# Optimization experiments

Hardware: AMD Instinct MI355X
Metric: run time of the kernel (lower is better)

The kernel has to match this reference:

```python
import jax, jax.numpy as jnp
import numpy as np

N_NODE, N_NET, E = 100000, 20000, 200000
H_NODE, H_NET, H_PIN = 64, 32, 16
O_NODE, O_NET = 32, 64


def setup_inputs() -> dict:
    key = jax.random.key(0)
    ks = jax.random.split(key, 8)
    return {
        'node_feat': jax.random.normal(ks[0], (N_NODE, H_NODE), jnp.float32),
        'net_feat': jax.random.normal(ks[1], (N_NET, H_NET), jnp.float32),
        'pin_feat': jax.random.normal(ks[2], (E, H_PIN), jnp.float32),
        'edge_node': jax.random.randint(ks[3], (E,), 0, N_NODE, jnp.int32),
        'edge_net': jax.random.randint(ks[4], (E,), 0, N_NET, jnp.int32),
        'W1': jax.random.normal(ks[5], (H_NODE, O_NET), jnp.float32) * 0.05,
        'b1': jnp.zeros((O_NET,), jnp.float32),
        'W2': jax.random.normal(ks[6], (H_PIN, H_NET * O_NODE), jnp.float32) * 0.05,
        'b2': jnp.zeros((H_NET * O_NODE,), jnp.float32),
        'b_nn': jnp.zeros((O_NODE,), jnp.float32),
    }


def reference(node_feat, net_feat, pin_feat, edge_node, edge_net, W1, b1, W2, b2, b_nn):
    ones = jnp.ones((E,), node_feat.dtype)
    # ---- relation 'pins': node -> net, DGL GraphConv with norm='both' ----
    out_deg = jnp.clip(jax.ops.segment_sum(ones, edge_node, num_segments=N_NODE), 1.0)  # src out-degree
    in_deg = jnp.clip(jax.ops.segment_sum(ones, edge_net, num_segments=N_NET), 1.0)     # dst in-degree
    src = node_feat * jax.lax.rsqrt(out_deg)[:, None]                                   # [N_node, H_node]
    agg = jax.ops.segment_sum(src[edge_node], edge_net, num_segments=N_NET)             # [N_net, H_node]
    net_out = (agg * jax.lax.rsqrt(in_deg)[:, None]) @ W1 + b1                           # [N_net, O_net]
    # ---- relation 'pinned': net -> node, DGL NNConv (mean aggregator) ----
    We = (pin_feat @ W2 + b2).reshape(E, H_NET, O_NODE)                                  # per-edge weight matrix
    msg = jnp.einsum('ei,eio->eo', net_feat[edge_net], We)                               # [E, O_node]
    node_deg = jnp.clip(jax.ops.segment_sum(ones, edge_node, num_segments=N_NODE), 1.0)
    node_out = jax.ops.segment_sum(msg, edge_node, num_segments=N_NODE) / node_deg[:, None] + b_nn
    return node_out, net_out
```

## Files before the change

kernel.cpp:

```cpp
#include <hip/hip_runtime.h>
#include <hip/hip_bf16.h>

#define N_NODE 100000
#define N_NET  20000
#define NE     200000
#define H_NODE 64
#define H_NET  32
#define H_PIN  16
#define O_NODE 32
#define O_NET  64
#define CSR_STRIDE 64


#define OFF_NETCNT  400000
#define OFF_CSR     480000
#define OFF_Z       10720000
#define OFF_C       51680000
#define ZERO_BYTES  480000

#define FILL_EDGE_BLKS 782
#define FILL_INIT_BLKS 3125

__global__ void k_fill(const int* __restrict__ en, const int* __restrict__ em,
                       int* __restrict__ node_deg, int* __restrict__ net_cnt,
                       int2* __restrict__ csr,
                       const float* __restrict__ b_nn,
                       float* __restrict__ out_node) {
    int t = threadIdx.x, b = blockIdx.x;
    if (b < FILL_EDGE_BLKS) {
        int e = b * 256 + t;
        if (e < NE) {
            int v = en[e], n = em[e];
            atomicAdd(&node_deg[v], 1);
            int slot = atomicAdd(&net_cnt[n], 1);
            csr[n * CSR_STRIDE + slot] = make_int2(e, v);
        }
        return;
    }
    int idx = (b - FILL_EDGE_BLKS) * 256 + t;
    float4 bb = ((const float4*)b_nn)[idx & 7];
    ((float4*)out_node)[idx] = bb;
}

#define ZNPB 16
__global__ void k_pre(const float* __restrict__ net_feat,
                      const float* __restrict__ W2, const float* __restrict__ b2,
                      float* __restrict__ Z, float* __restrict__ C) {
    __shared__ float sy[ZNPB][H_NET];
    int t = threadIdx.x;
    int base = blockIdx.x * ZNPB;
    for (int idx = t; idx < ZNPB * H_NET; idx += 256)
        sy[idx >> 5][idx & 31] = net_feat[(base + (idx >> 5)) * H_NET + (idx & 31)];
    __syncthreads();
    int o = t & 31, k4 = (t >> 5) & 3, rep = t >> 7;
    const float* w2p = W2 + (k4 * 4) * 1024 + o;
    float4 acc[8];
#pragma unroll
    for (int g = 0; g < 8; g++) acc[g] = make_float4(0.f, 0.f, 0.f, 0.f);
#pragma unroll 4
    for (int i = 0; i < H_NET; i++) {
        float w0 = w2p[0 * 1024 + i * 32];
        float w1 = w2p[1 * 1024 + i * 32];
        float w2v = w2p[2 * 1024 + i * 32];
        float w3 = w2p[3 * 1024 + i * 32];
#pragma unroll
        for (int g = 0; g < 8; g++) {
            float y = sy[rep * 8 + g][i];
            acc[g].x += w0 * y; acc[g].y += w1 * y;
            acc[g].z += w2v * y; acc[g].w += w3 * y;
        }
    }
#pragma unroll
    for (int g = 0; g < 8; g++) {
        int n = base + rep * 8 + g;
        *(float4*)&Z[(size_t)n * 512 + o * 16 + k4 * 4] = acc[g];
    }
#pragma unroll
    for (int r = 0; r < 2; r++) {
        int idx = t + r * 256;
        int g = idx >> 5, oo = idx & 31;
        float a = 0.f;
#pragma unroll
        for (int i = 0; i < H_NET; i++) a += sy[g][i] * b2[i * 32 + oo];
        C[(base + g) * 32 + oo] = a;
    }
}

__global__ void k_net(const float* __restrict__ node_feat,
                      const int* __restrict__ node_deg,
                      const int* __restrict__ net_cnt,
                      const int2* __restrict__ csr,
                      const float* __restrict__ W1,
                      const float* __restrict__ b1,
                      const float* __restrict__ Zg,
                      const float* __restrict__ Cg,
                      const float* __restrict__ pin_feat,
                      float* __restrict__ out_net, float* __restrict__ out_node) {
    __shared__ float  sW1[H_NODE * O_NET];
    __shared__ float  spin[4][32][16];
    __shared__ float4 srow4[4][16];
    int t = threadIdx.x;
    for (int i = t; i < 1024; i += 256)
        ((float4*)sW1)[i] = ((const float4*)W1)[i];

    int w = t >> 6, l = t & 63;
    int n = blockIdx.x * 4 + w;
    int beg = n * CSR_STRIDE, deg = net_cnt[n];
    int o = l & 31;
    int half = l >> 5;
    int q = l >> 4, f = l & 15;

    float4 z4[4];
    {
        const float4* zp = (const float4*)&Zg[(size_t)n * 512 + o * 16];
#pragma unroll
        for (int k4 = 0; k4 < 4; k4++) z4[k4] = zp[k4];
    }
    float c = Cg[n * 32 + o];

    const float4* nf4 = (const float4*)node_feat;
    const float4* pf4 = (const float4*)pin_feat;

    float4 acc4 = make_float4(0.f, 0.f, 0.f, 0.f);

    for (int j0 = 0; j0 < deg; j0 += 32) {
        int cnt = deg - j0; if (cnt > 32) cnt = 32;
        int vj = 0, ej = 0; float sj = 0.f;
        if (l < cnt) {
            int2 ev = csr[beg + j0 + l];
            ej = ev.x; vj = ev.y;
            float dv = (float)node_deg[vj]; if (dv < 1.f) dv = 1.f;
            sj = rsqrtf(dv);
        }
#pragma unroll
        for (int r = 0; r < 2; r++) {
            int jj = r * 16 + (l >> 2);
            int src = (jj < cnt) ? jj : cnt - 1;
            int e = __shfl(ej, src);
            float4 pv = pf4[(size_t)e * 4 + (l & 3)];
            ((float4*)&spin[w][jj][0])[l & 3] = pv;
        }
        int   vv[8]; float ss[8];
#pragma unroll
        for (int r = 0; r < 8; r++) {
            int jj = r * 4 + q;
            int src = (jj < cnt) ? jj : cnt - 1;
            vv[r] = __shfl(vj, src);
            float sv = __shfl(sj, src);
            ss[r] = (jj < cnt) ? sv : 0.f;
        }
        float4 xx[8];
#pragma unroll
        for (int r = 0; r < 8; r++) xx[r] = nf4[(size_t)vv[r] * 16 + f];
#pragma unroll
        for (int r = 0; r < 8; r++) {
            acc4.x += xx[r].x * ss[r];
            acc4.y += xx[r].y * ss[r];
            acc4.z += xx[r].z * ss[r];
            acc4.w += xx[r].w * ss[r];
        }
        for (int jj = 0; jj < cnt; jj += 2) {
            int je = jj + half;
            int src = (je < cnt) ? je : cnt - 1;
            int v = __shfl(vj, src);
            float sv = __shfl(sj, src);
            float inv = sv * sv;
            const float4* pr = (const float4*)&spin[w][src][0];
            float m = c;
#pragma unroll
            for (int k4 = 0; k4 < 4; k4++) {
                float4 pv = pr[k4];
                m += pv.x * z4[k4].x + pv.y * z4[k4].y
                   + pv.z * z4[k4].z + pv.w * z4[k4].w;
            }
            if (je < cnt) atomicAdd(&out_node[(size_t)v * O_NODE + o], m * inv);
        }
    }
    acc4.x += __shfl_xor(acc4.x, 16); acc4.y += __shfl_xor(acc4.y, 16);
    acc4.z += __shfl_xor(acc4.z, 16); acc4.w += __shfl_xor(acc4.w, 16);
    acc4.x += __shfl_xor(acc4.x, 32); acc4.y += __shfl_xor(acc4.y, 32);
    acc4.z += __shfl_xor(acc4.z, 32); acc4.w += __shfl_xor(acc4.w, 32);
    float dn = (deg < 1) ? 1.f : (float)deg;
    float rs = rsqrtf(dn);
    if (l < 16)
        srow4[w][l] = make_float4(acc4.x * rs, acc4.y * rs, acc4.z * rs, acc4.w * rs);
    __syncthreads();
    {
        const float* a = (const float*)&srow4[w][0];
        float oacc = b1[l];
#pragma unroll
        for (int h = 0; h < H_NODE; h++) oacc += a[h] * sW1[h * O_NET + l];
        out_net[n * O_NET + l] = oacc;
    }
}

extern "C" void kernel_launch(void* const* d_in, const int* in_sizes, int n_in,
                              void* d_out, int out_size, void* d_ws, size_t ws_size,
                              hipStream_t stream) {
    const float* node_feat = (const float*)d_in[0];
    const float* net_feat  = (const float*)d_in[1];
    const float* pin_feat  = (const float*)d_in[2];
    const int*   edge_node = (const int*)d_in[3];
    const int*   edge_net  = (const int*)d_in[4];
    const float* W1        = (const float*)d_in[5];
    const float* b1        = (const float*)d_in[6];
    const float* W2        = (const float*)d_in[7];
    const float* b2        = (const float*)d_in[8];
    const float* b_nn      = (const float*)d_in[9];

    float* out_node = (float*)d_out;
    float* out_net  = out_node + (size_t)N_NODE * O_NODE;

    char* ws = (char*)d_ws;
    int*   node_deg = (int*)ws;
    int*   net_cnt  = (int*)(ws + OFF_NETCNT);
    int2*  csr      = (int2*)(ws + OFF_CSR);
    float* Z        = (float*)(ws + OFF_Z);
    float* C        = (float*)(ws + OFF_C);

    (void)hipMemsetAsync(ws, 0, ZERO_BYTES, stream);

    k_fill<<<FILL_EDGE_BLKS + FILL_INIT_BLKS, 256, 0, stream>>>(
        edge_node, edge_net, node_deg, net_cnt, csr, b_nn, out_node);

    k_pre<<<N_NET / ZNPB, 256, 0, stream>>>(net_feat, W2, b2, Z, C);

    k_net<<<N_NET / 4, 256, 0, stream>>>(
        node_feat, node_deg, net_cnt, csr,
        W1, b1, Z, C, pin_feat, out_net, out_node);
}
```

Measured before the change: 174.0 us.

## Fuse precompute into build kernel, store Z in bf16, trim W1 staging and gathers

Merges the Z/C precompute kernel into the CSR build kernel so one launch does all setup work. The per-net Z matrix is stored in bf16, halving its write and read traffic, which costs some precision in the per-edge messages. k_net drops the shared-memory staging of W1 and reads it directly from global memory. It also skips the second half of the pin and node gathers when a net has 16 or fewer edges.

New measurement: 163.7 us. -5.9%, faster.

```diff
diff --git a/kernel.cpp b/kernel.cpp
--- a/kernel.cpp
+++ b/kernel.cpp
@@ -15,75 +15,87 @@
 #define OFF_NETCNT  400000
 #define OFF_CSR     480000
 #define OFF_Z       10720000
-#define OFF_C       51680000
+#define OFF_C       31200000
 #define ZERO_BYTES  480000
 
-#define FILL_EDGE_BLKS 782
-#define FILL_INIT_BLKS 3125
-
-__global__ void k_fill(const int* __restrict__ en, const int* __restrict__ em,
-                       int* __restrict__ node_deg, int* __restrict__ net_cnt,
-                       int2* __restrict__ csr,
-                       const float* __restrict__ b_nn,
-                       float* __restrict__ out_node) {
+static __device__ __forceinline__ unsigned short f2bf(float f) {
+    unsigned int u = __float_as_uint(f);
+    u += 0x7fff + ((u >> 16) & 1);
+    return (unsigned short)(u >> 16);
+}
+static __device__ __forceinline__ float bf2f(unsigned short h) {
+    return __uint_as_float(((unsigned int)h) << 16);
+}
+
+#define BLD_EDGE_BLKS 782
+#define BLD_Z_BLKS    1250
+#define BLD_INIT_BLKS 3125
+#define ZNPB 16
+
+__global__ void k_build(const int* __restrict__ en, const int* __restrict__ em,
+                        int* __restrict__ node_deg, int* __restrict__ net_cnt,
+                        int2* __restrict__ csr,
+                        const float* __restrict__ net_feat,
+                        const float* __restrict__ W2, const float* __restrict__ b2,
+                        unsigned short* __restrict__ Zb, float* __restrict__ C,
+                        const float* __restrict__ b_nn,
+                        float* __restrict__ out_node) {
     int t = threadIdx.x, b = blockIdx.x;
-    if (b < FILL_EDGE_BLKS) {
+    if (b < BLD_EDGE_BLKS) {
         int e = b * 256 + t;
         if (e < NE) {
             int v = en[e], n = em[e];
             atomicAdd(&node_deg[v], 1);
             int slot = atomicAdd(&net_cnt[n], 1);
-            csr[n * CSR_STRIDE + slot] = make_int2(e, v);
+            if (slot < CSR_STRIDE) csr[n * CSR_STRIDE + slot] = make_int2(e, v);
         }
         return;
     }
-    int idx = (b - FILL_EDGE_BLKS) * 256 + t;
-    float4 bb = ((const float4*)b_nn)[idx & 7];
-    ((float4*)out_node)[idx] = bb;
-}
-
-#define ZNPB 16
-__global__ void k_pre(const float* __restrict__ net_feat,
-                      const float* __restrict__ W2, const float* __restrict__ b2,
-                      float* __restrict__ Z, float* __restrict__ C) {
-    __shared__ float sy[ZNPB][H_NET];
-    int t = threadIdx.x;
-    int base = blockIdx.x * ZNPB;
-    for (int idx = t; idx < ZNPB * H_NET; idx += 256)
-        sy[idx >> 5][idx & 31] = net_feat[(base + (idx >> 5)) * H_NET + (idx & 31)];
-    __syncthreads();
-    int o = t & 31, k4 = (t >> 5) & 3, rep = t >> 7;
-    const float* w2p = W2 + (k4 * 4) * 1024 + o;
-    float4 acc[8];
-#pragma unroll
-    for (int g = 0; g < 8; g++) acc[g] = make_float4(0.f, 0.f, 0.f, 0.f);
+    if (b < BLD_EDGE_BLKS + BLD_Z_BLKS) {
+        __shared__ float sy[ZNPB][H_NET];
+        int base = (b - BLD_EDGE_BLKS) * ZNPB;
+        for (int idx = t; idx < ZNPB * H_NET; idx += 256)
+            sy[idx >> 5][idx & 31] = net_feat[(base + (idx >> 5)) * H_NET + (idx & 31)];
+        __syncthreads();
+        int o = t & 31, k4 = (t >> 5) & 3, rep = t >> 7;
+        const float* w2p = W2 + (k4 * 4) * 1024 + o;
+        float4 acc[8];
+#pragma unroll
+        for (int g = 0; g < 8; g++) acc[g] = make_float4(0.f, 0.f, 0.f, 0.f);
 #pragma unroll 4
-    for (int i = 0; i < H_NET; i++) {
-        float w0 = w2p[0 * 1024 + i * 32];
-        float w1 = w2p[1 * 1024 + i * 32];
-        float w2v = w2p[2 * 1024 + i * 32];
-        float w3 = w2p[3 * 1024 + i * 32];
+        for (int i = 0; i < H_NET; i++) {
+            float w0 = w2p[0 * 1024 + i * 32];
+            float w1 = w2p[1 * 1024 + i * 32];
+            float w2v = w2p[2 * 1024 + i * 32];
+            float w3 = w2p[3 * 1024 + i * 32];
+#pragma unroll
+            for (int g = 0; g < 8; g++) {
+                float y = sy[rep * 8 + g][i];
+                acc[g].x += w0 * y; acc[g].y += w1 * y;
+                acc[g].z += w2v * y; acc[g].w += w3 * y;
+            }
+        }
 #pragma unroll
         for (int g = 0; g < 8; g++) {
-            float y = sy[rep * 8 + g][i];
-            acc[g].x += w0 * y; acc[g].y += w1 * y;
-            acc[g].z += w2v * y; acc[g].w += w3 * y;
-        }
-    }
-#pragma unroll
-    for (int g = 0; g < 8; g++) {
-        int n = base + rep * 8 + g;
-        *(float4*)&Z[(size_t)n * 512 + o * 16 + k4 * 4] = acc[g];
-    }
-#pragma unroll
-    for (int r = 0; r < 2; r++) {
-        int idx = t + r * 256;
-        int g = idx >> 5, oo = idx & 31;
-        float a = 0.f;
-#pragma unroll
-        for (int i = 0; i < H_NET; i++) a += sy[g][i] * b2[i * 32 + oo];
-        C[(base + g) * 32 + oo] = a;
-    }
+            int n = base + rep * 8 + g;
+            ushort4 uz;
+            uz.x = f2bf(acc[g].x); uz.y = f2bf(acc[g].y);
+            uz.z = f2bf(acc[g].z); uz.w = f2bf(acc[g].w);
+            *(ushort4*)&Zb[(size_t)n * 512 + o * 16 + k4 * 4] = uz;
+        }
+#pragma unroll
+        for (int r = 0; r < 2; r++) {
+            int idx = t + r * 256;
+            int g = idx >> 5, oo = idx & 31;
+            float a = 0.f;
+#pragma unroll
+            for (int i = 0; i < H_NET; i++) a += sy[g][i] * b2[i * 32 + oo];
+            C[(base + g) * 32 + oo] = a;
+        }
+        return;
+    }
+    int idx = (b - BLD_EDGE_BLKS - BLD_Z_BLKS) * 256 + t;
+    ((float4*)out_node)[idx] = ((const float4*)b_nn)[idx & 7];
 }
 
 __global__ void k_net(const float* __restrict__ node_feat,
@@ -92,17 +104,13 @@
                       const int2* __restrict__ csr,
                       const float* __restrict__ W1,
                       const float* __restrict__ b1,
-                      const float* __restrict__ Zg,
+                      const unsigned short* __restrict__ Zb,
                       const float* __restrict__ Cg,
                       const float* __restrict__ pin_feat,
                       float* __restrict__ out_net, float* __restrict__ out_node) {
-    __shared__ float  sW1[H_NODE * O_NET];
     __shared__ float  spin[4][32][16];
     __shared__ float4 srow4[4][16];
     int t = threadIdx.x;
-    for (int i = t; i < 1024; i += 256)
-        ((float4*)sW1)[i] = ((const float4*)W1)[i];
-
     int w = t >> 6, l = t & 63;
     int n = blockIdx.x * 4 + w;
     int beg = n * CSR_STRIDE, deg = net_cnt[n];
@@ -110,11 +118,16 @@
     int half = l >> 5;
     int q = l >> 4, f = l & 15;
 
-    float4 z4[4];
+    float z[16];
     {
-        const float4* zp = (const float4*)&Zg[(size_t)n * 512 + o * 16];
-#pragma unroll
-        for (int k4 = 0; k4 < 4; k4++) z4[k4] = zp[k4];
+        const uint4* zp = (const uint4*)&Zb[(size_t)n * 512 + o * 16];
+        uint4 za = zp[0], zb = zp[1];
+        unsigned int uu[8] = {za.x, za.y, za.z, za.w, zb.x, zb.y, zb.z, zb.w};
+#pragma unroll
+        for (int i = 0; i < 8; i++) {
+            z[2 * i]     = bf2f((unsigned short)(uu[i] & 0xffffu));
+            z[2 * i + 1] = bf2f((unsigned short)(uu[i] >> 16));
+        }
     }
     float c = Cg[n * 32 + o];
 
@@ -132,32 +145,57 @@
             float dv = (float)node_deg[vj]; if (dv < 1.f) dv = 1.f;
             sj = rsqrtf(dv);
         }
-#pragma unroll
-        for (int r = 0; r < 2; r++) {
-            int jj = r * 16 + (l >> 2);
+        {
+            int jj = l >> 2;
             int src = (jj < cnt) ? jj : cnt - 1;
             int e = __shfl(ej, src);
             float4 pv = pf4[(size_t)e * 4 + (l & 3)];
             ((float4*)&spin[w][jj][0])[l & 3] = pv;
         }
-        int   vv[8]; float ss[8];
-#pragma unroll
-        for (int r = 0; r < 8; r++) {
-            int jj = r * 4 + q;
+        if (cnt > 16) {
+            int jj = 16 + (l >> 2);
             int src = (jj < cnt) ? jj : cnt - 1;
-            vv[r] = __shfl(vj, src);
-            float sv = __shfl(sj, src);
-            ss[r] = (jj < cnt) ? sv : 0.f;
-        }
-        float4 xx[8];
-#pragma unroll
-        for (int r = 0; r < 8; r++) xx[r] = nf4[(size_t)vv[r] * 16 + f];
-#pragma unroll
-        for (int r = 0; r < 8; r++) {
-            acc4.x += xx[r].x * ss[r];
-            acc4.y += xx[r].y * ss[r];
-            acc4.z += xx[r].z * ss[r];
-            acc4.w += xx[r].w * ss[r];
+            int e = __shfl(ej, src);
+            float4 pv = pf4[(size_t)e * 4 + (l & 3)];
+            ((float4*)&spin[w][jj][0])[l & 3] = pv;
+        }
+        {
+            int vv[4]; float ss[4];
+#pragma unroll
+            for (int r = 0; r < 4; r++) {
+                int jj = r * 4 + q;
+                int src = (jj < cnt) ? jj : cnt - 1;
+                vv[r] = __shfl(vj, src);
+                float sv = __shfl(sj, src);
+                ss[r] = (jj < cnt) ? sv : 0.f;
+            }
+            float4 xx[4];
+#pragma unroll
+            for (int r = 0; r < 4; r++) xx[r] = nf4[(size_t)vv[r] * 16 + f];
+#pragma unroll
+            for (int r = 0; r < 4; r++) {
+                acc4.x += xx[r].x * ss[r]; acc4.y += xx[r].y * ss[r];
+                acc4.z += xx[r].z * ss[r]; acc4.w += xx[r].w * ss[r];
+            }
+        }
+        if (cnt > 16) {
+            int vv[4]; float ss[4];
+#pragma unroll
+            for (int r = 0; r < 4; r++) {
+                int jj = 16 + r * 4 + q;
+                int src = (jj < cnt) ? jj : cnt - 1;
+                vv[r] = __shfl(vj, src);
+                float sv = __shfl(sj, src);
+                ss[r] = (jj < cnt) ? sv : 0.f;
+            }
+            float4 xx[4];
+#pragma unroll
+            for (int r = 0; r < 4; r++) xx[r] = nf4[(size_t)vv[r] * 16 + f];
+#pragma unroll
+            for (int r = 0; r < 4; r++) {
+                acc4.x += xx[r].x * ss[r]; acc4.y += xx[r].y * ss[r];
+                acc4.z += xx[r].z * ss[r]; acc4.w += xx[r].w * ss[r];
+            }
         }
         for (int jj = 0; jj < cnt; jj += 2) {
             int je = jj + half;
@@ -170,8 +208,8 @@
 #pragma unroll
             for (int k4 = 0; k4 < 4; k4++) {
                 float4 pv = pr[k4];
-                m += pv.x * z4[k4].x + pv.y * z4[k4].y
-                   + pv.z * z4[k4].z + pv.w * z4[k4].w;
+                m += pv.x * z[k4 * 4 + 0] + pv.y * z[k4 * 4 + 1]
+                   + pv.z * z[k4 * 4 + 2] + pv.w * z[k4 * 4 + 3];
             }
             if (je < cnt) atomicAdd(&out_node[(size_t)v * O_NODE + o], m * inv);
         }
@@ -188,8 +226,8 @@
     {
         const float* a = (const float*)&srow4[w][0];
         float oacc = b1[l];
-#pragma unroll
-        for (int h = 0; h < H_NODE; h++) oacc += a[h] * sW1[h * O_NET + l];
+#pragma unroll 16
+        for (int h = 0; h < H_NODE; h++) oacc += a[h] * W1[h * O_NET + l];
         out_net[n * O_NET + l] = oacc;
     }
 }
@@ -212,20 +250,19 @@
     float* out_net  = out_node + (size_t)N_NODE * O_NODE;
 
     char* ws = (char*)d_ws;
-    int*   node_deg = (int*)ws;
-    int*   net_cnt  = (int*)(ws + OFF_NETCNT);
-    int2*  csr      = (int2*)(ws + OFF_CSR);
-    float* Z        = (float*)(ws + OFF_Z);
-    float* C        = (float*)(ws + OFF_C);
+    int*            node_deg = (int*)ws;
+    int*            net_cnt  = (int*)(ws + OFF_NETCNT);
+    int2*           csr      = (int2*)(ws + OFF_CSR);
+    unsigned short* Zb       = (unsigned short*)(ws + OFF_Z);
+    float*          C        = (float*)(ws + OFF_C);
 
     (void)hipMemsetAsync(ws, 0, ZERO_BYTES, stream);
 
-    k_fill<<<FILL_EDGE_BLKS + FILL_INIT_BLKS, 256, 0, stream>>>(
-        edge_node, edge_net, node_deg, net_cnt, csr, b_nn, out_node);
-
-    k_pre<<<N_NET / ZNPB, 256, 0, stream>>>(net_feat, W2, b2, Z, C);
+    k_build<<<BLD_EDGE_BLKS + BLD_Z_BLKS + BLD_INIT_BLKS, 256, 0, stream>>>(
+        edge_node, edge_net, node_deg, net_cnt, csr,
+        net_feat, W2, b2, Zb, C, b_nn, out_node);
 
     k_net<<<N_NET / 4, 256, 0, stream>>>(
         node_feat, node_deg, net_cnt, csr,
-        W1, b1, Z, C, pin_feat, out_net, out_node);
-}
+        W1, b1, Zb, C, pin_feat, out_net, out_node);
+}
```
